# Kernel tuning notes

Measured on AMD Instinct MI355X. Metric: run time of the kernel, lower is better.

The kernel has to match this reference:

```python
import jax, jax.numpy as jnp
import numpy as np

P, N, GRID, C, S, STEPS, N_ADJ = 128, 512, 112, 64, 128, 3, 4
HW = GRID * GRID
IN_DIM = C + 2


def _ring_adjacency():
    # prepare_gcn_component builds a ring graph: each vertex connected to
    # n_adj nearest neighbors along the polygon, row-normalized.
    offs = np.concatenate([np.arange(1, N_ADJ // 2 + 1), -np.arange(1, N_ADJ // 2 + 1)])
    A = np.zeros((N, N), np.float32)
    idx = np.arange(N)
    for o in offs:
        A[idx, (idx + o) % N] = 1.0
    A /= A.sum(1, keepdims=True)
    return jnp.asarray(A)


def setup_inputs() -> dict:
    key = jax.random.key(0)
    ks = jax.random.split(key, 10)
    std = 0.01  # matches m.weight.data.normal_(0.0, 0.01)
    return {
        "feature": jax.random.normal(ks[0], (P, HW, C), jnp.float32),
        "init_polys": jax.random.uniform(ks[1], (P, N, 2), jnp.float32),
        "adj": _ring_adjacency(),
        "W1s": jax.random.normal(ks[2], (STEPS, IN_DIM, S), jnp.float32) * std,
        "W1n": jax.random.normal(ks[3], (STEPS, IN_DIM, S), jnp.float32) * std,
        "b1": jnp.zeros((STEPS, S), jnp.float32),
        "W2s": jax.random.normal(ks[4], (STEPS, S, S), jnp.float32) * std,
        "W2n": jax.random.normal(ks[5], (STEPS, S, S), jnp.float32) * std,
        "b2": jnp.zeros((STEPS, S), jnp.float32),
        "Wfc": jax.random.normal(ks[6], (STEPS, S, 2), jnp.float32) * std,
        "bfc": jnp.zeros((STEPS, 2), jnp.float32),
    }


def _gather(feat, ids):
    # feat: [P, HW, C], ids: [P, N] int -> [P, N, C]
    return jnp.take_along_axis(feat, ids[:, :, None], axis=1)


def _nearest_sample(feature, poly):
    # step-0 `sampling` path: gather at floor(coord*grid) flat indices
    X0 = jnp.clip(jnp.floor(poly[..., 0] * GRID), 0, GRID - 1)
    Y0 = jnp.clip(jnp.floor(poly[..., 1] * GRID), 0, GRID - 1)
    ids = (X0 + Y0 * GRID).astype(jnp.int32)
    return _gather(feature, ids)


def _interpolated_sum(feature, poly):
    Xs = poly[..., 0] * GRID
    Ys = poly[..., 1] * GRID
    X0 = jnp.floor(Xs); X1 = X0 + 1.0
    Y0 = jnp.floor(Ys); Y1 = Y0 + 1.0
    w00 = (X1 - Xs) * (Y1 - Ys)
    w01 = (X1 - Xs) * (Ys - Y0)
    w10 = (Xs - X0) * (Y1 - Ys)
    w11 = (Xs - X0) * (Ys - Y0)
    X0c = jnp.clip(X0, 0, GRID - 1).astype(jnp.int32)
    X1c = jnp.clip(X1, 0, GRID - 1).astype(jnp.int32)
    Y0c = jnp.clip(Y0, 0, GRID - 1).astype(jnp.int32)
    Y1c = jnp.clip(Y1, 0, GRID - 1).astype(jnp.int32)
    M00 = _gather(feature, X0c + Y0c * GRID)
    M01 = _gather(feature, X0c + Y1c * GRID)
    M10 = _gather(feature, X1c + Y0c * GRID)
    M11 = _gather(feature, X1c + Y1c * GRID)
    return (w00[..., None] * M00 + w01[..., None] * M01 +
            w10[..., None] * M10 + w11[..., None] * M11)


def _gconv(x, adj, Ws, Wn, b):
    # x: [P, N, D]; adj: [N, N] (shared ring graph)
    nbr = jnp.einsum('nm,pmd->pnd', adj, x)
    return x @ Ws + nbr @ Wn + b


def _gcn(x, adj, i, W1s, W1n, b1, W2s, W2n, b2, Wfc, bfc):
    h = jax.nn.relu(_gconv(x, adj, W1s[i], W1n[i], b1[i]))
    h = jax.nn.relu(_gconv(h, adj, W2s[i], W2n[i], b2[i]))
    return h @ Wfc[i] + bfc[i]  # [P, N, 2]


def reference(feature, init_polys, adj, W1s, W1n, b1, W2s, W2n, b2, Wfc, bfc):
    poly = init_polys
    for i in range(STEPS):
        cnn_feat = _nearest_sample(feature, poly) if i == 0 else _interpolated_sum(feature, poly)
        inp = jnp.concatenate([cnn_feat, poly], axis=2)  # [P, N, C+2]
        pred = _gcn(inp, adj, i, W1s, W1n, b1, W2s, W2n, b2, Wfc, bfc)
        poly = poly + pred
    return poly
```

## Files before the change

kernel.cpp:

```cpp
#include <hip/hip_runtime.h>

#define P_      128
#define NV      512
#define GRID_   112
#define HW_     (GRID_*GRID_)
#define C_      64
#define S_      128

typedef short bf16x8 __attribute__((ext_vector_type(8)));
typedef float f32x4  __attribute__((ext_vector_type(4)));

__device__ __forceinline__ unsigned short f2bf(float x) {
    union { float f; unsigned int u; } v; v.f = x;
    unsigned int r = (v.u + 0x7FFFu + ((v.u >> 16) & 1u)) >> 16;
    return (unsigned short)r;
}
__device__ __forceinline__ float2 up2(unsigned int u) {
    union { unsigned int u; float f; } a, b;
    a.u = u << 16; b.u = u & 0xFFFF0000u;
    return make_float2(a.f, b.f);
}
__device__ __forceinline__ unsigned int pk2(float lo, float hi) {
    return (unsigned int)f2bf(lo) | ((unsigned int)f2bf(hi) << 16);
}

__global__ __launch_bounds__(256) void wprep_kernel(
    const float* __restrict__ W1s, const float* __restrict__ W1n,
    const float* __restrict__ W2s, const float* __restrict__ W2n,
    unsigned short* __restrict__ W1p, unsigned short* __restrict__ W2p)
{
    int idx = blockIdx.x * 256 + threadIdx.x;
    const int N1 = 3 * 5 * 8 * 64 * 8;
    const int N2 = 3 * 8 * 8 * 64 * 8;
    if (idx < N1) {
        int j = idx & 7, lane = (idx >> 3) & 63, nt = (idx >> 9) & 7;
        int ks = (idx >> 12) % 5, step = idx / 20480;
        int n = nt * 16 + (lane & 15);
        int k = ks * 32 + (lane >> 4) * 8 + j;
        float v = 0.f;
        if (k < 66)       v = W1s[(step * 66 + k) * 128 + n];
        else if (k < 132) v = W1n[(step * 66 + (k - 66)) * 128 + n];
        W1p[idx] = f2bf(v);
    } else if (idx < N1 + N2) {
        int e = idx - N1;
        int j = e & 7, lane = (e >> 3) & 63, nt = (e >> 9) & 7;
        int ks = (e >> 12) & 7, step = e >> 15;
        int n = nt * 16 + (lane & 15);
        int k = ks * 32 + (lane >> 4) * 8 + j;
        float v = (k < 128) ? W2s[(step * 128 + k) * 128 + n]
                            : W2n[(step * 128 + (k - 128)) * 128 + n];
        W2p[e] = f2bf(v);
    }
}

__global__ __launch_bounds__(256) void gcn_kernel(
    const float* __restrict__ feature,
    const unsigned short* __restrict__ W1p,
    const float* __restrict__ b1,
    const unsigned short* __restrict__ W2p,
    const float* __restrict__ b2,
    const float* __restrict__ Wfc, const float* __restrict__ bfc,
    const float* __restrict__ poly_in, float* __restrict__ poly_out,
    int nearest)
{
    __shared__ __align__(16) char smem[54400];
    unsigned short* rawS  = (unsigned short*)smem;
    unsigned int*   raw_u = (unsigned int*)smem;
    unsigned int*   A1_u  = (unsigned int*)(smem + 10368);
    unsigned short* h1s   = (unsigned short*)smem;
    unsigned int*   A2_u  = (unsigned int*)(smem + 21120);
    float*          h2    = (float*)(smem + 21120);

    int p = blockIdx.x >> 3, n0 = (blockIdx.x & 7) * 64;
    int wv = threadIdx.x >> 6, lane = threadIdx.x & 63;
    int m = lane & 15, q = lane >> 4;
    int nt0 = wv * 2;

    const float* fb    = feature + (size_t)p * HW_ * C_;
    const float* pbase = poly_in + (size_t)p * NV * 2;
    #pragma unroll 3
    for (int r = wv; r < 72; r += 4) {
        int vtx = (n0 + r - 4) & (NV - 1);
        float px = pbase[2 * vtx], py = pbase[2 * vtx + 1];
        float val;
        if (nearest) {
            float X0 = fminf(fmaxf(floorf(px * (float)GRID_), 0.f), (float)(GRID_ - 1));
            float Y0 = fminf(fmaxf(floorf(py * (float)GRID_), 0.f), (float)(GRID_ - 1));
            int id = (int)X0 + (int)Y0 * GRID_;
            val = fb[(size_t)id * C_ + lane];
        } else {
            float Xs = px * (float)GRID_, Ys = py * (float)GRID_;
            float X0 = floorf(Xs), Y0 = floorf(Ys);
            float X1 = X0 + 1.f, Y1 = Y0 + 1.f;
            float ax = X1 - Xs, bx = Xs - X0;
            float ay = Y1 - Ys, by = Ys - Y0;
            int X0c = (int)fminf(fmaxf(X0, 0.f), (float)(GRID_ - 1));
            int X1c = (int)fminf(fmaxf(X1, 0.f), (float)(GRID_ - 1));
            int Y0c = (int)fminf(fmaxf(Y0, 0.f), (float)(GRID_ - 1));
            int Y1c = (int)fminf(fmaxf(Y1, 0.f), (float)(GRID_ - 1));
            float m00 = fb[(size_t)(X0c + Y0c * GRID_) * C_ + lane];
            float m01 = fb[(size_t)(X0c + Y1c * GRID_) * C_ + lane];
            float m10 = fb[(size_t)(X1c + Y0c * GRID_) * C_ + lane];
            float m11 = fb[(size_t)(X1c + Y1c * GRID_) * C_ + lane];
            val = (ax * ay) * m00 + (ax * by) * m01 + (bx * ay) * m10 + (bx * by) * m11;
        }
        unsigned short* row = rawS + r * 72;
        row[lane] = f2bf(val);
        if (lane < 8)
            row[64 + lane] = (lane == 0) ? f2bf(px) : (lane == 1) ? f2bf(py)
                                                                  : (unsigned short)0;
    }
    __syncthreads();

    for (int idx = threadIdx.x; idx < 80 * 84; idx += 256) {
        int a = idx / 84, u = idx - a * 84;
        unsigned int val = 0u;
        if (a < 68) {
            if (u < 33) {
                val = raw_u[(a + 2) * 36 + u];
            } else if (u < 66) {
                int uu = u - 33;
                float2 fa = up2(raw_u[a * 36 + uu]),       fb2 = up2(raw_u[(a + 1) * 36 + uu]);
                float2 fc = up2(raw_u[(a + 3) * 36 + uu]), fd  = up2(raw_u[(a + 4) * 36 + uu]);
                val = pk2(0.25f * (fa.x + fb2.x + fc.x + fd.x),
                          0.25f * (fa.y + fb2.y + fc.y + fd.y));
            }
        }
        A1_u[idx] = val;
    }
    __syncthreads();

    f32x4 acc1[5][2];
    #pragma unroll
    for (int i = 0; i < 5; i++) {
        acc1[i][0] = (f32x4){0.f, 0.f, 0.f, 0.f};
        acc1[i][1] = (f32x4){0.f, 0.f, 0.f, 0.f};
    }
    const bf16x8* B1 = (const bf16x8*)W1p;
    const unsigned short* A1s = (const unsigned short*)A1_u;
    #pragma unroll
    for (int ks = 0; ks < 5; ks++) {
        bf16x8 bfr0 = B1[(ks * 8 + nt0) * 64 + lane];
        bf16x8 bfr1 = B1[(ks * 8 + nt0 + 1) * 64 + lane];
        #pragma unroll
        for (int mt = 0; mt < 5; mt++) {
            bf16x8 a = *(const bf16x8*)(A1s + (mt * 16 + m) * 168 + ks * 32 + q * 8);
            acc1[mt][0] = __builtin_amdgcn_mfma_f32_16x16x32_bf16(a, bfr0, acc1[mt][0], 0, 0, 0);
            acc1[mt][1] = __builtin_amdgcn_mfma_f32_16x16x32_bf16(a, bfr1, acc1[mt][1], 0, 0, 0);
        }
    }
    __syncthreads();

    #pragma unroll
    for (int mt = 0; mt < 5; mt++) {
        #pragma unroll
        for (int j = 0; j < 2; j++) {
            int col = (nt0 + j) * 16 + m;
            float bias = b1[col];
            #pragma unroll
            for (int rg = 0; rg < 4; rg++) {
                int row = mt * 16 + q * 4 + rg;
                h1s[row * 132 + col] = f2bf(fmaxf(acc1[mt][j][rg] + bias, 0.f));
            }
        }
    }
    __syncthreads();

    const unsigned int* h1u = (const unsigned int*)h1s;
    for (int idx = threadIdx.x; idx < 64 * 128; idx += 256) {
        int a = idx >> 7, u = idx & 127;
        unsigned int val;
        if (u < 64) {
            val = h1u[(a + 2) * 66 + u];
        } else {
            int uu = u - 64;
            float2 fa = up2(h1u[a * 66 + uu]),       fb2 = up2(h1u[(a + 1) * 66 + uu]);
            float2 fc = up2(h1u[(a + 3) * 66 + uu]), fd  = up2(h1u[(a + 4) * 66 + uu]);
            val = pk2(0.25f * (fa.x + fb2.x + fc.x + fd.x),
                      0.25f * (fa.y + fb2.y + fc.y + fd.y));
        }
        A2_u[a * 130 + u] = val;
    }
    __syncthreads();

    f32x4 acc2[4][2];
    #pragma unroll
    for (int i = 0; i < 4; i++) {
        acc2[i][0] = (f32x4){0.f, 0.f, 0.f, 0.f};
        acc2[i][1] = (f32x4){0.f, 0.f, 0.f, 0.f};
    }
    const bf16x8* B2 = (const bf16x8*)W2p;
    const unsigned short* A2s = (const unsigned short*)A2_u;
    #pragma unroll
    for (int ks = 0; ks < 8; ks++) {
        bf16x8 bfr0 = B2[(ks * 8 + nt0) * 64 + lane];
        bf16x8 bfr1 = B2[(ks * 8 + nt0 + 1) * 64 + lane];
        #pragma unroll
        for (int mt = 0; mt < 4; mt++) {
            bf16x8 a = *(const bf16x8*)(A2s + (mt * 16 + m) * 260 + ks * 32 + q * 8);
            acc2[mt][0] = __builtin_amdgcn_mfma_f32_16x16x32_bf16(a, bfr0, acc2[mt][0], 0, 0, 0);
            acc2[mt][1] = __builtin_amdgcn_mfma_f32_16x16x32_bf16(a, bfr1, acc2[mt][1], 0, 0, 0);
        }
    }
    __syncthreads();

    #pragma unroll
    for (int mt = 0; mt < 4; mt++) {
        #pragma unroll
        for (int j = 0; j < 2; j++) {
            int col = (nt0 + j) * 16 + m;
            float bias = b2[col];
            #pragma unroll
            for (int rg = 0; rg < 4; rg++) {
                int row = mt * 16 + q * 4 + rg;
                h2[row * 129 + col] = fmaxf(acc2[mt][j][rg] + bias, 0.f);
            }
        }
    }
    __syncthreads();

    {
        int t = threadIdx.x;
        int oi = t >> 1, half = t & 1;
        int v = oi >> 1, j = oi & 1;
        float pr = half ? 0.f : bfc[j];
        const float* hv = h2 + v * 129 + half * 64;
        #pragma unroll 8
        for (int cc = 0; cc < 64; cc++)
            pr += hv[cc] * Wfc[(half * 64 + cc) * 2 + j];
        pr += __shfl_xor(pr, 1);
        if (half == 0) {
            size_t o = ((size_t)p * NV + n0 + v) * 2 + j;
            poly_out[o] = poly_in[o] + pr;
        }
    }
}

extern "C" void kernel_launch(void* const* d_in, const int* in_sizes, int n_in,
                              void* d_out, int out_size, void* d_ws, size_t ws_size,
                              hipStream_t stream)
{
    const float* feature    = (const float*)d_in[0];
    const float* init_polys = (const float*)d_in[1];
    const float* W1s = (const float*)d_in[3];
    const float* W1n = (const float*)d_in[4];
    const float* b1  = (const float*)d_in[5];
    const float* W2s = (const float*)d_in[6];
    const float* W2n = (const float*)d_in[7];
    const float* b2  = (const float*)d_in[8];
    const float* Wfc = (const float*)d_in[9];
    const float* bfc = (const float*)d_in[10];
    float* out = (float*)d_out;

    char* wsb = (char*)d_ws;
    float* polyA = (float*)wsb;                  wsb += (size_t)P_ * NV * 2 * 4;
    float* polyB = (float*)wsb;                  wsb += (size_t)P_ * NV * 2 * 4;
    unsigned short* W1p = (unsigned short*)wsb;  wsb += (size_t)61440 * 2;
    unsigned short* W2p = (unsigned short*)wsb;

    wprep_kernel<<<624, 256, 0, stream>>>(W1s, W1n, W2s, W2n, W1p, W2p);

    const float* pin = init_polys;
    for (int i = 0; i < 3; i++) {
        float* pout = (i == 2) ? out : ((i == 0) ? polyA : polyB);
        gcn_kernel<<<P_ * 8, 256, 0, stream>>>(
            feature,
            W1p + (size_t)i * 20480, b1 + i * 128,
            W2p + (size_t)i * 32768, b2 + i * 128,
            Wfc + i * 256, bfc + i * 2,
            pin, pout, i == 0);
        pin = pout;
    }
}
```

Baseline: 692.6 us.

## Split feature sampling into separate kernel and shrink GCN shared memory

Moves the bilinear/nearest feature gather into its own kernel that writes bf16 rows to a workspace buffer, so each vertex is sampled once instead of being recomputed as a halo by neighbouring blocks. The GCN kernel now only copies its rows into shared memory. It reads the layer-2 self operand straight from h1 instead of copying it, which cuts shared memory from about 54KB to 38KB, and adds a launch bound of 4 blocks for occupancy. The final FC dot product is split across four accumulators. The cost is an extra launch per step and a global round trip for the sampled features.

```diff
diff --git a/kernel.cpp b/kernel.cpp
--- a/kernel.cpp
+++ b/kernel.cpp
@@ -53,62 +53,69 @@
     }
 }
 
-__global__ __launch_bounds__(256) void gcn_kernel(
-    const float* __restrict__ feature,
+__global__ __launch_bounds__(256) void sample_kernel(
+    const float* __restrict__ feature, const float* __restrict__ poly,
+    unsigned short* __restrict__ inp, int nearest)
+{
+    int w = threadIdx.x >> 6, lane = threadIdx.x & 63;
+    int g = blockIdx.x * 4 + w;
+    int p = g >> 9;
+    float px = poly[2 * g], py = poly[2 * g + 1];
+    const float* fb = feature + (size_t)p * HW_ * C_;
+    float val;
+    if (nearest) {
+        float X0 = fminf(fmaxf(floorf(px * (float)GRID_), 0.f), (float)(GRID_ - 1));
+        float Y0 = fminf(fmaxf(floorf(py * (float)GRID_), 0.f), (float)(GRID_ - 1));
+        int id = (int)X0 + (int)Y0 * GRID_;
+        val = fb[(size_t)id * C_ + lane];
+    } else {
+        float Xs = px * (float)GRID_, Ys = py * (float)GRID_;
+        float X0 = floorf(Xs), Y0 = floorf(Ys);
+        float X1 = X0 + 1.f, Y1 = Y0 + 1.f;
+        float ax = X1 - Xs, bx = Xs - X0;
+        float ay = Y1 - Ys, by = Ys - Y0;
+        int X0c = (int)fminf(fmaxf(X0, 0.f), (float)(GRID_ - 1));
+        int X1c = (int)fminf(fmaxf(X1, 0.f), (float)(GRID_ - 1));
+        int Y0c = (int)fminf(fmaxf(Y0, 0.f), (float)(GRID_ - 1));
+        int Y1c = (int)fminf(fmaxf(Y1, 0.f), (float)(GRID_ - 1));
+        float m00 = fb[(size_t)(X0c + Y0c * GRID_) * C_ + lane];
+        float m01 = fb[(size_t)(X0c + Y1c * GRID_) * C_ + lane];
+        float m10 = fb[(size_t)(X1c + Y0c * GRID_) * C_ + lane];
+        float m11 = fb[(size_t)(X1c + Y1c * GRID_) * C_ + lane];
+        val = (ax * ay) * m00 + (ax * by) * m01 + (bx * ay) * m10 + (bx * by) * m11;
+    }
+    unsigned short* row = inp + (size_t)g * 72;
+    row[lane] = f2bf(val);
+    if (lane < 8)
+        row[64 + lane] = (lane == 0) ? f2bf(px) : (lane == 1) ? f2bf(py) : 0;
+}
+
+__global__ __launch_bounds__(256, 4) void gcn_kernel(
+    const unsigned short* __restrict__ inp,
     const unsigned short* __restrict__ W1p,
     const float* __restrict__ b1,
     const unsigned short* __restrict__ W2p,
     const float* __restrict__ b2,
     const float* __restrict__ Wfc, const float* __restrict__ bfc,
-    const float* __restrict__ poly_in, float* __restrict__ poly_out,
-    int nearest)
-{
-    __shared__ __align__(16) char smem[54400];
-    unsigned short* rawS  = (unsigned short*)smem;
+    const float* __restrict__ poly_in, float* __restrict__ poly_out)
+{
+    __shared__ __align__(16) char smem[38016];
     unsigned int*   raw_u = (unsigned int*)smem;
     unsigned int*   A1_u  = (unsigned int*)(smem + 10368);
     unsigned short* h1s   = (unsigned short*)smem;
-    unsigned int*   A2_u  = (unsigned int*)(smem + 21120);
-    float*          h2    = (float*)(smem + 21120);
+    unsigned int*   R2_u  = (unsigned int*)(smem + 21120);
+    float*          h2    = (float*)smem;
 
     int p = blockIdx.x >> 3, n0 = (blockIdx.x & 7) * 64;
     int wv = threadIdx.x >> 6, lane = threadIdx.x & 63;
     int m = lane & 15, q = lane >> 4;
     int nt0 = wv * 2;
 
-    const float* fb    = feature + (size_t)p * HW_ * C_;
-    const float* pbase = poly_in + (size_t)p * NV * 2;
-    #pragma unroll 3
-    for (int r = wv; r < 72; r += 4) {
-        int vtx = (n0 + r - 4) & (NV - 1);
-        float px = pbase[2 * vtx], py = pbase[2 * vtx + 1];
-        float val;
-        if (nearest) {
-            float X0 = fminf(fmaxf(floorf(px * (float)GRID_), 0.f), (float)(GRID_ - 1));
-            float Y0 = fminf(fmaxf(floorf(py * (float)GRID_), 0.f), (float)(GRID_ - 1));
-            int id = (int)X0 + (int)Y0 * GRID_;
-            val = fb[(size_t)id * C_ + lane];
-        } else {
-            float Xs = px * (float)GRID_, Ys = py * (float)GRID_;
-            float X0 = floorf(Xs), Y0 = floorf(Ys);
-            float X1 = X0 + 1.f, Y1 = Y0 + 1.f;
-            float ax = X1 - Xs, bx = Xs - X0;
-            float ay = Y1 - Ys, by = Ys - Y0;
-            int X0c = (int)fminf(fmaxf(X0, 0.f), (float)(GRID_ - 1));
-            int X1c = (int)fminf(fmaxf(X1, 0.f), (float)(GRID_ - 1));
-            int Y0c = (int)fminf(fmaxf(Y0, 0.f), (float)(GRID_ - 1));
-            int Y1c = (int)fminf(fmaxf(Y1, 0.f), (float)(GRID_ - 1));
-            float m00 = fb[(size_t)(X0c + Y0c * GRID_) * C_ + lane];
-            float m01 = fb[(size_t)(X0c + Y1c * GRID_) * C_ + lane];
-            float m10 = fb[(size_t)(X1c + Y0c * GRID_) * C_ + lane];
-            float m11 = fb[(size_t)(X1c + Y1c * GRID_) * C_ + lane];
-            val = (ax * ay) * m00 + (ax * by) * m01 + (bx * ay) * m10 + (bx * by) * m11;
-        }
-        unsigned short* row = rawS + r * 72;
-        row[lane] = f2bf(val);
-        if (lane < 8)
-            row[64 + lane] = (lane == 0) ? f2bf(px) : (lane == 1) ? f2bf(py)
-                                                                  : (unsigned short)0;
+    const uint4* inp4 = (const uint4*)(inp + (size_t)p * NV * 72);
+    uint4* raw4 = (uint4*)smem;
+    for (int idx = threadIdx.x; idx < 72 * 9; idx += 256) {
+        int r = idx / 9, u = idx - r * 9;
+        raw4[idx] = inp4[(size_t)((n0 + r - 4) & 511) * 9 + u];
     }
     __syncthreads();
 
@@ -167,19 +174,12 @@
     __syncthreads();
 
     const unsigned int* h1u = (const unsigned int*)h1s;
-    for (int idx = threadIdx.x; idx < 64 * 128; idx += 256) {
-        int a = idx >> 7, u = idx & 127;
-        unsigned int val;
-        if (u < 64) {
-            val = h1u[(a + 2) * 66 + u];
-        } else {
-            int uu = u - 64;
-            float2 fa = up2(h1u[a * 66 + uu]),       fb2 = up2(h1u[(a + 1) * 66 + uu]);
-            float2 fc = up2(h1u[(a + 3) * 66 + uu]), fd  = up2(h1u[(a + 4) * 66 + uu]);
-            val = pk2(0.25f * (fa.x + fb2.x + fc.x + fd.x),
-                      0.25f * (fa.y + fb2.y + fc.y + fd.y));
-        }
-        A2_u[a * 130 + u] = val;
+    for (int idx = threadIdx.x; idx < 64 * 64; idx += 256) {
+        int a = idx >> 6, u = idx & 63;
+        float2 fa = up2(h1u[a * 66 + u]),       fb2 = up2(h1u[(a + 1) * 66 + u]);
+        float2 fc = up2(h1u[(a + 3) * 66 + u]), fd  = up2(h1u[(a + 4) * 66 + u]);
+        R2_u[a * 66 + u] = pk2(0.25f * (fa.x + fb2.x + fc.x + fd.x),
+                               0.25f * (fa.y + fb2.y + fc.y + fd.y));
     }
     __syncthreads();
 
@@ -190,14 +190,18 @@
         acc2[i][1] = (f32x4){0.f, 0.f, 0.f, 0.f};
     }
     const bf16x8* B2 = (const bf16x8*)W2p;
-    const unsigned short* A2s = (const unsigned short*)A2_u;
+    const unsigned short* selfS = h1s + 2 * 132;
+    const unsigned short* ringS = (const unsigned short*)R2_u;
     #pragma unroll
     for (int ks = 0; ks < 8; ks++) {
         bf16x8 bfr0 = B2[(ks * 8 + nt0) * 64 + lane];
         bf16x8 bfr1 = B2[(ks * 8 + nt0 + 1) * 64 + lane];
         #pragma unroll
         for (int mt = 0; mt < 4; mt++) {
-            bf16x8 a = *(const bf16x8*)(A2s + (mt * 16 + m) * 260 + ks * 32 + q * 8);
+            const unsigned short* ap = (ks < 4)
+                ? selfS + (mt * 16 + m) * 132 + ks * 32 + q * 8
+                : ringS + (mt * 16 + m) * 132 + (ks - 4) * 32 + q * 8;
+            bf16x8 a = *(const bf16x8*)ap;
             acc2[mt][0] = __builtin_amdgcn_mfma_f32_16x16x32_bf16(a, bfr0, acc2[mt][0], 0, 0, 0);
             acc2[mt][1] = __builtin_amdgcn_mfma_f32_16x16x32_bf16(a, bfr1, acc2[mt][1], 0, 0, 0);
         }
@@ -223,11 +227,17 @@
         int t = threadIdx.x;
         int oi = t >> 1, half = t & 1;
         int v = oi >> 1, j = oi & 1;
-        float pr = half ? 0.f : bfc[j];
         const float* hv = h2 + v * 129 + half * 64;
-        #pragma unroll 8
-        for (int cc = 0; cc < 64; cc++)
-            pr += hv[cc] * Wfc[(half * 64 + cc) * 2 + j];
+        const float* wf = Wfc + half * 128 + j;
+        float s0 = 0.f, s1 = 0.f, s2 = 0.f, s3 = 0.f;
+        #pragma unroll
+        for (int cc = 0; cc < 64; cc += 4) {
+            s0 += hv[cc]     * wf[2 * cc];
+            s1 += hv[cc + 1] * wf[2 * cc + 2];
+            s2 += hv[cc + 2] * wf[2 * cc + 4];
+            s3 += hv[cc + 3] * wf[2 * cc + 6];
+        }
+        float pr = (s0 + s1) + (s2 + s3) + (half ? 0.f : bfc[j]);
         pr += __shfl_xor(pr, 1);
         if (half == 0) {
             size_t o = ((size_t)p * NV + n0 + v) * 2 + j;
@@ -256,19 +266,20 @@
     float* polyA = (float*)wsb;                  wsb += (size_t)P_ * NV * 2 * 4;
     float* polyB = (float*)wsb;                  wsb += (size_t)P_ * NV * 2 * 4;
     unsigned short* W1p = (unsigned short*)wsb;  wsb += (size_t)61440 * 2;
-    unsigned short* W2p = (unsigned short*)wsb;
+    unsigned short* W2p = (unsigned short*)wsb;  wsb += (size_t)98304 * 2;
+    unsigned short* inp = (unsigned short*)wsb;
 
     wprep_kernel<<<624, 256, 0, stream>>>(W1s, W1n, W2s, W2n, W1p, W2p);
 
     const float* pin = init_polys;
     for (int i = 0; i < 3; i++) {
         float* pout = (i == 2) ? out : ((i == 0) ? polyA : polyB);
+        sample_kernel<<<P_ * NV / 4, 256, 0, stream>>>(feature, pin, inp, i == 0);
         gcn_kernel<<<P_ * 8, 256, 0, stream>>>(
-            feature,
-            W1p + (size_t)i * 20480, b1 + i * 128,
+            inp, W1p + (size_t)i * 20480, b1 + i * 128,
             W2p + (size_t)i * 32768, b2 + i * 128,
             Wfc + i * 256, bfc + i * 2,
-            pin, pout, i == 0);
+            pin, pout);
         pin = pout;
     }
 }
```

After: 623.3 us. -10.0%, faster.
